# Performance work log

Measured on AMD Instinct MI355X. Metric: run time of the kernel, lower is better.

Reference implementation:

```python
import jax, jax.numpy as jnp
import numpy as np

B, T, INPUT, HIDDEN = 64, 512, 512, 1024

def setup_inputs() -> dict:
    key = jax.random.key(0)
    ks = jax.random.split(key, 5)
    s_x = 1.0 / np.sqrt(INPUT)
    s_h = 1.0 / np.sqrt(HIDDEN)
    return {
        "x": jax.random.normal(ks[0], (B, T, INPUT), dtype=jnp.float32),
        "h_0": jnp.zeros((B, HIDDEN), dtype=jnp.float32),
        "Wx": jax.random.uniform(ks[1], (HIDDEN, INPUT), jnp.float32, -s_x, s_x),
        "bx": jax.random.uniform(ks[2], (HIDDEN,), jnp.float32, -s_x, s_x),
        "Wh": jax.random.uniform(ks[3], (HIDDEN, HIDDEN), jnp.float32, -s_h, s_h),
        "bh": jax.random.uniform(ks[4], (HIDDEN,), jnp.float32, -s_h, s_h),
    }

def reference(x, h_0, Wx, bx, Wh, bh):
    # Precompute input projection for all timesteps as one big GEMM: [B,T,H]
    x_proj = jnp.einsum('bti,hi->bth', x, Wx) + bx

    def step(h, xp_t):
        # pre-activation output stored; activated value carried forward (faithful to source)
        pre = xp_t + h @ Wh.T + bh        # [B,H]
        h_next = jnp.tanh(pre)
        return h_next, pre

    # scan over time: xs has leading T axis
    h_final, outs = jax.lax.scan(step, h_0, jnp.swapaxes(x_proj, 0, 1))
    outputs = jnp.swapaxes(outs, 0, 1)    # [B,T,H]
    return outputs, h_final
```

## Files before the change

### kernel.cpp

```cpp
#include <hip/hip_runtime.h>
#include <stdint.h>


typedef __attribute__((ext_vector_type(8))) short bf16x8;
typedef __attribute__((ext_vector_type(4))) float f32x4;

__device__ __forceinline__ uint32_t f2bf(float f) {
    union { float f; uint32_t u; } v; v.f = f;
    return (v.u + 0x7FFFu + ((v.u >> 16) & 1u)) >> 16;
}
__device__ __forceinline__ uint32_t pack2bf(float a, float b) {
    return f2bf(a) | (f2bf(b) << 16);
}
__device__ __forceinline__ float fast_tanh(float x) {
    const float xc = fminf(fmaxf(x, -15.f), 15.f);
    const float e  = __expf(2.f * xc);
    return (e - 1.f) * __builtin_amdgcn_rcpf(e + 1.f);
}

__global__ __launch_bounds__(256) void xproj_gemm(
    const float* __restrict__ x, const float* __restrict__ Wx,
    const float* __restrict__ bx, const float* __restrict__ bh,
    float* __restrict__ out)
{
    __shared__ __align__(16) uint8_t Ab[128 * 128];
    __shared__ __align__(16) uint8_t Bb[128 * 128];

    const int tid  = threadIdx.x;
    const int lane = tid & 63;
    const int wid  = tid >> 6;
    const int wm = wid >> 1, wn = wid & 1;
    const int m0 = (int)(blockIdx.x >> 3) * 128;
    const int n0 = (int)(blockIdx.x & 7) * 128;

    f32x4 acc[4][4];
    #pragma unroll
    for (int i = 0; i < 4; ++i)
        #pragma unroll
        for (int j = 0; j < 4; ++j) acc[i][j] = (f32x4){0.f, 0.f, 0.f, 0.f};

    const int sr = tid >> 4;
    const int sk = (tid & 15) << 2;

    for (int k0 = 0; k0 < 512; k0 += 64) {
        __syncthreads();
        #pragma unroll
        for (int p = 0; p < 8; ++p) {
            const int r = sr + p * 16;
            const float4 a = *(const float4*)(x  + (size_t)(m0 + r) * 512 + k0 + sk);
            const float4 b = *(const float4*)(Wx + (size_t)(n0 + r) * 512 + k0 + sk);
            const int byo = r * 128 + ((sk << 1) ^ ((r & 7) << 4));
            *(uint2*)(Ab + byo) = make_uint2(pack2bf(a.x, a.y), pack2bf(a.z, a.w));
            *(uint2*)(Bb + byo) = make_uint2(pack2bf(b.x, b.y), pack2bf(b.z, b.w));
        }
        __syncthreads();
        #pragma unroll
        for (int kt = 0; kt < 2; ++kt) {
            bf16x8 af[4], bfr[4];
            const int kb = (kt << 6) + ((lane >> 4) << 4);
            #pragma unroll
            for (int q = 0; q < 4; ++q) {
                const int ar = wm * 64 + q * 16 + (lane & 15);
                const int br = wn * 64 + q * 16 + (lane & 15);
                af[q]  = *(const bf16x8*)(Ab + ar * 128 + (kb ^ ((ar & 7) << 4)));
                bfr[q] = *(const bf16x8*)(Bb + br * 128 + (kb ^ ((br & 7) << 4)));
            }
            #pragma unroll
            for (int mt = 0; mt < 4; ++mt)
                #pragma unroll
                for (int nt = 0; nt < 4; ++nt)
                    acc[mt][nt] = __builtin_amdgcn_mfma_f32_16x16x32_bf16(
                        af[mt], bfr[nt], acc[mt][nt], 0, 0, 0);
        }
    }

    #pragma unroll
    for (int nt = 0; nt < 4; ++nt) {
        const int n = n0 + wn * 64 + nt * 16 + (lane & 15);
        const float bias = bx[n] + bh[n];
        #pragma unroll
        for (int mt = 0; mt < 4; ++mt) {
            const int mb = m0 + wm * 64 + mt * 16 + ((lane >> 4) << 2);
            #pragma unroll
            for (int i = 0; i < 4; ++i)
                out[(size_t)(mb + i) * 1024 + n] = acc[mt][nt][i] + bias;
        }
    }
}

__global__ __launch_bounds__(512, 1) void rnn_scan(
    const float* __restrict__ h0, const float* __restrict__ Wh,
    float* __restrict__ out, float* __restrict__ hfin,
    uint32_t* __restrict__ hbuf)
{
    __shared__ __align__(16) uint8_t htile[2][49152];

    const int tid  = threadIdx.x;
    const int lane = tid & 63;
    const int wid  = tid >> 6;
    const int g    = (int)blockIdx.x & 7;
    const int nb   = (int)blockIdx.x >> 3;
    const int gb0  = g * 8;
    const int col  = nb * 128 + wid * 16 + (lane & 15);
    const int r4b  = ((lane >> 4) & 1) << 2;

    bf16x8 whf[32];
    {
        const float* wp = Wh + (size_t)col * 1024 + ((lane >> 4) << 3);
        #pragma unroll
        for (int kt = 0; kt < 32; ++kt) {
            const float4 w0 = *(const float4*)(wp + kt * 32);
            const float4 w1 = *(const float4*)(wp + kt * 32 + 4);
            bf16x8 f;
            f[0] = (short)f2bf(w0.x); f[1] = (short)f2bf(w0.y);
            f[2] = (short)f2bf(w0.z); f[3] = (short)f2bf(w0.w);
            f[4] = (short)f2bf(w1.x); f[5] = (short)f2bf(w1.y);
            f[6] = (short)f2bf(w1.z); f[7] = (short)f2bf(w1.w);
            whf[kt] = f;
        }
    }

    {
        const int colI = nb * 128 + lane * 2;
        const uint32_t u0 = f2bf(h0[(size_t)(gb0 + wid) * 1024 + colI]);
        const uint32_t u1 = f2bf(h0[(size_t)(gb0 + wid) * 1024 + colI + 1]);
        const int idx = (gb0 + wid) * 1024 + colI;
        __hip_atomic_store(&hbuf[idx],     (u0 << 16) | 1u, __ATOMIC_RELAXED, __HIP_MEMORY_SCOPE_AGENT);
        __hip_atomic_store(&hbuf[idx + 1], (u1 << 16) | 1u, __ATOMIC_RELAXED, __HIP_MEMORY_SCOPE_AGENT);
        *(uint32_t*)(htile[0] + wid * 2048 + ((colI * 2) ^ (wid << 4))) = u0 | (u1 << 16);
    }

    const int pb  = wid;
    const int pc0 = lane * 2;
    int ridx[7];
    #pragma unroll
    for (int r = 0; r < 7; ++r) {
        const int rbk = (nb + 1 + r) & 7;
        ridx[r] = (gb0 + pb) * 1024 + rbk * 128 + pc0;
    }

    float xpv[4];
    #pragma unroll
    for (int i = 0; i < 4; ++i)
        xpv[i] = out[((size_t)(gb0 + r4b + i) * 512 + 0) * 1024 + col];

    for (int t = 0; t < 512; ++t) {
        const int cur = t & 1;
        uint32_t* const src = hbuf + cur * 65536;
        uint32_t* const dst = hbuf + (cur ^ 1) * 65536;
        const uint32_t exptag = (uint32_t)(t + 1);
        const uint32_t ntag   = exptag + 1;

        uint32_t v[14];
        int rounds = 0;
        while (true) {
            #pragma unroll
            for (int r = 0; r < 7; ++r) {
                v[2 * r]     = __hip_atomic_load(&src[ridx[r]],     __ATOMIC_RELAXED, __HIP_MEMORY_SCOPE_AGENT);
                v[2 * r + 1] = __hip_atomic_load(&src[ridx[r] + 1], __ATOMIC_RELAXED, __HIP_MEMORY_SCOPE_AGENT);
            }
            bool ok = true;
            #pragma unroll
            for (int p = 0; p < 14; ++p) ok &= ((v[p] & 0xFFFFu) == exptag);
            if (ok) break;
            if (++rounds > 256) __builtin_amdgcn_s_sleep(2);
        }
        #pragma unroll
        for (int r = 0; r < 7; ++r) {
            const int rbk = (nb + 1 + r) & 7;
            const int c0  = rbk * 128 + pc0;
            const uint32_t pk = (v[2 * r] >> 16) | (v[2 * r + 1] & 0xFFFF0000u);
            *(uint32_t*)(htile[cur] + pb * 2048 + ((c0 * 2) ^ (pb << 4))) = pk;
        }
        __syncthreads();

        float xnext[4];
        if (t < 511) {
            #pragma unroll
            for (int i = 0; i < 4; ++i)
                xnext[i] = out[((size_t)(gb0 + r4b + i) * 512 + (t + 1)) * 1024 + col];
        }

        f32x4 a0 = (f32x4){0.f,0.f,0.f,0.f}, a1 = a0, a2 = a0, a3 = a0;
        {
            const int b_  = lane & 7;
            const int kbx = (lane >> 4) << 4;
            const int swz = b_ << 4;
            const uint8_t* hb = htile[cur] + b_ * 2048;
            #pragma unroll
            for (int kt = 0; kt < 32; kt += 4) {
                const bf16x8 f0 = *(const bf16x8*)(hb + (((kt    ) * 64 + kbx) ^ swz));
                const bf16x8 f1 = *(const bf16x8*)(hb + (((kt + 1) * 64 + kbx) ^ swz));
                const bf16x8 f2 = *(const bf16x8*)(hb + (((kt + 2) * 64 + kbx) ^ swz));
                const bf16x8 f3 = *(const bf16x8*)(hb + (((kt + 3) * 64 + kbx) ^ swz));
                a0 = __builtin_amdgcn_mfma_f32_16x16x32_bf16(f0, whf[kt    ], a0, 0, 0, 0);
                a1 = __builtin_amdgcn_mfma_f32_16x16x32_bf16(f1, whf[kt + 1], a1, 0, 0, 0);
                a2 = __builtin_amdgcn_mfma_f32_16x16x32_bf16(f2, whf[kt + 2], a2, 0, 0, 0);
                a3 = __builtin_amdgcn_mfma_f32_16x16x32_bf16(f3, whf[kt + 3], a3, 0, 0, 0);
            }
        }

        float pre[4], hn[4];
        #pragma unroll
        for (int i = 0; i < 4; ++i) {
            pre[i] = ((a0[i] + a1[i]) + (a2[i] + a3[i])) + xpv[i];
            hn[i]  = fast_tanh(pre[i]);
        }
        if (lane < 32) {
            if (t < 511) {
                uint32_t hu[4];
                #pragma unroll
                for (int i = 0; i < 4; ++i) hu[i] = f2bf(hn[i]);
                #pragma unroll
                for (int i = 0; i < 4; ++i)
                    __hip_atomic_store(&dst[(gb0 + r4b + i) * 1024 + col], (hu[i] << 16) | ntag,
                                       __ATOMIC_RELAXED, __HIP_MEMORY_SCOPE_AGENT);
                #pragma unroll
                for (int i = 0; i < 4; ++i)
                    *(uint16_t*)(htile[cur ^ 1] + (r4b + i) * 2048 + ((col * 2) ^ ((r4b + i) << 4))) = (uint16_t)hu[i];
            }
        } else {
            #pragma unroll
            for (int i = 0; i < 4; ++i) {
                out[((size_t)(gb0 + r4b + i) * 512 + t) * 1024 + col] = pre[i];
                if (t == 511) hfin[(size_t)(gb0 + r4b + i) * 1024 + col] = hn[i];
            }
        }
        #pragma unroll
        for (int i = 0; i < 4; ++i) xpv[i] = xnext[i];
    }
}

extern "C" void kernel_launch(void* const* d_in, const int* in_sizes, int n_in,
                              void* d_out, int out_size, void* d_ws, size_t ws_size,
                              hipStream_t stream) {
    const float* x   = (const float*)d_in[0];
    const float* h0_ = (const float*)d_in[1];
    const float* Wx  = (const float*)d_in[2];
    const float* bx  = (const float*)d_in[3];
    const float* Wh  = (const float*)d_in[4];
    const float* bh  = (const float*)d_in[5];
    float* out  = (float*)d_out;
    float* hfin = out + (size_t)64 * 512 * 1024;
    uint32_t* hbuf = (uint32_t*)d_ws;

    hipMemsetAsync(d_ws, 0xFF, (size_t)2 * 64 * 1024 * sizeof(uint32_t), stream);

    xproj_gemm<<<dim3(2048), dim3(256), 0, stream>>>(x, Wx, bx, bh, out);
    rnn_scan<<<dim3(64), dim3(512), 0, stream>>>(h0_, Wh, out, hfin, hbuf);
}
```

Before: 1.562 ms.

## Remap h-exchange polling to per-wave column blocks with 64-bit loads

Changes how each wave polls the tagged hidden-state buffer. Each non-zero wave now owns one remote column block across 8 batch rows and reads it with eight 64-bit atomic loads per lane, replacing 14 scattered 32-bit loads per lane. Wave 0, whose block is local, skips polling. A double-buffered load/check loop keeps one round of loads in flight while the previous round's tags are checked, to cut spin latency. The lane-to-data mapping is more complex, and wrong indexing or tag masking would produce incorrect results or deadlock.

```diff
diff --git a/kernel.cpp b/kernel.cpp
--- a/kernel.cpp
+++ b/kernel.cpp
@@ -4,6 +4,7 @@
 
 typedef __attribute__((ext_vector_type(8))) short bf16x8;
 typedef __attribute__((ext_vector_type(4))) float f32x4;
+typedef unsigned long long u64;
 
 __device__ __forceinline__ uint32_t f2bf(float f) {
     union { float f; uint32_t u; } v; v.f = f;
@@ -130,14 +131,13 @@
         *(uint32_t*)(htile[0] + wid * 2048 + ((colI * 2) ^ (wid << 4))) = u0 | (u1 << 16);
     }
 
-    const int pb  = wid;
-    const int pc0 = lane * 2;
-    int ridx[7];
-    #pragma unroll
-    for (int r = 0; r < 7; ++r) {
-        const int rbk = (nb + 1 + r) & 7;
-        ridx[r] = (gb0 + pb) * 1024 + rbk * 128 + pc0;
-    }
+    const int rbk = (nb + wid) & 7;
+    const int bl  = lane >> 3;
+    const int c8  = (lane & 7) << 4;
+    const int ib  = (gb0 + bl) * 1024 + rbk * 128 + c8;
+    const int sbase = bl * 2048;
+    const int soff  = rbk * 256 + ((lane & 7) << 5);
+    const int sxor  = bl << 4;
 
     float xpv[4];
     #pragma unroll
@@ -150,27 +150,45 @@
         uint32_t* const dst = hbuf + (cur ^ 1) * 65536;
         const uint32_t exptag = (uint32_t)(t + 1);
         const uint32_t ntag   = exptag + 1;
-
-        uint32_t v[14];
-        int rounds = 0;
-        while (true) {
-            #pragma unroll
-            for (int r = 0; r < 7; ++r) {
-                v[2 * r]     = __hip_atomic_load(&src[ridx[r]],     __ATOMIC_RELAXED, __HIP_MEMORY_SCOPE_AGENT);
-                v[2 * r + 1] = __hip_atomic_load(&src[ridx[r] + 1], __ATOMIC_RELAXED, __HIP_MEMORY_SCOPE_AGENT);
-            }
-            bool ok = true;
-            #pragma unroll
-            for (int p = 0; p < 14; ++p) ok &= ((v[p] & 0xFFFFu) == exptag);
-            if (ok) break;
-            if (++rounds > 256) __builtin_amdgcn_s_sleep(2);
-        }
-        #pragma unroll
-        for (int r = 0; r < 7; ++r) {
-            const int rbk = (nb + 1 + r) & 7;
-            const int c0  = rbk * 128 + pc0;
-            const uint32_t pk = (v[2 * r] >> 16) | (v[2 * r + 1] & 0xFFFF0000u);
-            *(uint32_t*)(htile[cur] + pb * 2048 + ((c0 * 2) ^ (pb << 4))) = pk;
+        const u64 tag2 = ((u64)exptag << 32) | (u64)exptag;
+
+        if (wid > 0) {
+            u64 va[8], vb[8];
+            #pragma unroll
+            for (int j = 0; j < 8; ++j)
+                va[j] = __hip_atomic_load((const u64*)&src[ib + 2 * j],
+                                          __ATOMIC_RELAXED, __HIP_MEMORY_SCOPE_AGENT);
+            const u64* w = va;
+            int rounds = 0;
+            while (true) {
+                #pragma unroll
+                for (int j = 0; j < 8; ++j)
+                    vb[j] = __hip_atomic_load((const u64*)&src[ib + 2 * j],
+                                              __ATOMIC_RELAXED, __HIP_MEMORY_SCOPE_AGENT);
+                bool ok = true;
+                #pragma unroll
+                for (int j = 0; j < 8; ++j)
+                    ok &= (((va[j] ^ tag2) & 0x0000FFFF0000FFFFull) == 0);
+                if (ok) { w = va; break; }
+
+                #pragma unroll
+                for (int j = 0; j < 8; ++j)
+                    va[j] = __hip_atomic_load((const u64*)&src[ib + 2 * j],
+                                              __ATOMIC_RELAXED, __HIP_MEMORY_SCOPE_AGENT);
+                ok = true;
+                #pragma unroll
+                for (int j = 0; j < 8; ++j)
+                    ok &= (((vb[j] ^ tag2) & 0x0000FFFF0000FFFFull) == 0);
+                if (ok) { w = vb; break; }
+                if (++rounds > 512) __builtin_amdgcn_s_sleep(2);
+            }
+            #pragma unroll
+            for (int j = 0; j < 8; ++j) {
+                const uint32_t lo = (uint32_t)w[j];
+                const uint32_t hi = (uint32_t)(w[j] >> 32);
+                const uint32_t pk = (lo >> 16) | (hi & 0xFFFF0000u);
+                *(uint32_t*)(htile[cur] + sbase + ((soff + 4 * j) ^ sxor)) = pk;
+            }
         }
         __syncthreads();
 
```

New measurement: 3.705 ms. +137.2%, slower.

## Add per-block flag polling before loading tagged hidden-state values

Applied to the files above, without the earlier changes.

Each block now publishes one flag per step after all of its tagged hidden-state stores have drained (waitcnt plus a block barrier). Consumers spin on seven per-producer flags, one per lane, instead of repeatedly reloading fourteen tagged data words, then read the data once and keep the tag check as a fallback. The next-step xproj prefetch moves after the output stores. The aim is lighter polling traffic on the critical cross-block handoff, at the cost of an extra barrier and a memory drain on every step.

```diff
diff --git a/kernel.cpp b/kernel.cpp
--- a/kernel.cpp
+++ b/kernel.cpp
@@ -91,7 +91,8 @@
 __global__ __launch_bounds__(512, 1) void rnn_scan(
     const float* __restrict__ h0, const float* __restrict__ Wh,
     float* __restrict__ out, float* __restrict__ hfin,
-    uint32_t* __restrict__ hbuf)
+    uint32_t* __restrict__ hbuf,
+    uint32_t* __restrict__ tagb)
 {
     __shared__ __align__(16) uint8_t htile[2][49152];
 
@@ -128,6 +129,11 @@
         __hip_atomic_store(&hbuf[idx],     (u0 << 16) | 1u, __ATOMIC_RELAXED, __HIP_MEMORY_SCOPE_AGENT);
         __hip_atomic_store(&hbuf[idx + 1], (u1 << 16) | 1u, __ATOMIC_RELAXED, __HIP_MEMORY_SCOPE_AGENT);
         *(uint32_t*)(htile[0] + wid * 2048 + ((colI * 2) ^ (wid << 4))) = u0 | (u1 << 16);
+        asm volatile("s_waitcnt vmcnt(0)" ::: "memory");
+        __syncthreads();
+        if (tid == 0)
+            __hip_atomic_store(&tagb[((0 << 6) + (g << 3) + nb) << 4], 1u,
+                               __ATOMIC_RELAXED, __HIP_MEMORY_SCOPE_AGENT);
     }
 
     const int pb  = wid;
@@ -138,6 +144,8 @@
         const int rbk = (nb + 1 + r) & 7;
         ridx[r] = (gb0 + pb) * 1024 + rbk * 128 + pc0;
     }
+    const int myrbk  = (nb + 1 + (lane < 7 ? lane : 0)) & 7;
+    const int tbase  = ((g << 3) + myrbk) << 4;
 
     float xpv[4];
     #pragma unroll
@@ -151,19 +159,38 @@
         const uint32_t exptag = (uint32_t)(t + 1);
         const uint32_t ntag   = exptag + 1;
 
+        {
+            const uint32_t* tp = &tagb[(cur << 10) + tbase];
+            int rounds = 0;
+            while (true) {
+                uint32_t tv = exptag;
+                if (lane < 7)
+                    tv = __hip_atomic_load(tp, __ATOMIC_RELAXED, __HIP_MEMORY_SCOPE_AGENT);
+                if (__all(tv == exptag)) break;
+                if (++rounds > 256) __builtin_amdgcn_s_sleep(2);
+            }
+        }
+
         uint32_t v[14];
-        int rounds = 0;
-        while (true) {
+        {
             #pragma unroll
             for (int r = 0; r < 7; ++r) {
                 v[2 * r]     = __hip_atomic_load(&src[ridx[r]],     __ATOMIC_RELAXED, __HIP_MEMORY_SCOPE_AGENT);
                 v[2 * r + 1] = __hip_atomic_load(&src[ridx[r] + 1], __ATOMIC_RELAXED, __HIP_MEMORY_SCOPE_AGENT);
             }
-            bool ok = true;
-            #pragma unroll
-            for (int p = 0; p < 14; ++p) ok &= ((v[p] & 0xFFFFu) == exptag);
-            if (ok) break;
-            if (++rounds > 256) __builtin_amdgcn_s_sleep(2);
+            int rounds = 0;
+            while (true) {
+                bool ok = true;
+                #pragma unroll
+                for (int p = 0; p < 14; ++p) ok &= ((v[p] & 0xFFFFu) == exptag);
+                if (ok) break;
+                #pragma unroll
+                for (int r = 0; r < 7; ++r) {
+                    v[2 * r]     = __hip_atomic_load(&src[ridx[r]],     __ATOMIC_RELAXED, __HIP_MEMORY_SCOPE_AGENT);
+                    v[2 * r + 1] = __hip_atomic_load(&src[ridx[r] + 1], __ATOMIC_RELAXED, __HIP_MEMORY_SCOPE_AGENT);
+                }
+                if (++rounds > 256) __builtin_amdgcn_s_sleep(2);
+            }
         }
         #pragma unroll
         for (int r = 0; r < 7; ++r) {
@@ -173,13 +200,6 @@
             *(uint32_t*)(htile[cur] + pb * 2048 + ((c0 * 2) ^ (pb << 4))) = pk;
         }
         __syncthreads();
-
-        float xnext[4];
-        if (t < 511) {
-            #pragma unroll
-            for (int i = 0; i < 4; ++i)
-                xnext[i] = out[((size_t)(gb0 + r4b + i) * 512 + (t + 1)) * 1024 + col];
-        }
 
         f32x4 a0 = (f32x4){0.f,0.f,0.f,0.f}, a1 = a0, a2 = a0, a3 = a0;
         {
@@ -206,8 +226,8 @@
             pre[i] = ((a0[i] + a1[i]) + (a2[i] + a3[i])) + xpv[i];
             hn[i]  = fast_tanh(pre[i]);
         }
-        if (lane < 32) {
-            if (t < 511) {
+        if (t < 511) {
+            if (lane < 32) {
                 uint32_t hu[4];
                 #pragma unroll
                 for (int i = 0; i < 4; ++i) hu[i] = f2bf(hn[i]);
@@ -219,15 +239,27 @@
                 for (int i = 0; i < 4; ++i)
                     *(uint16_t*)(htile[cur ^ 1] + (r4b + i) * 2048 + ((col * 2) ^ ((r4b + i) << 4))) = (uint16_t)hu[i];
             }
-        } else {
+            asm volatile("s_waitcnt vmcnt(0)" ::: "memory");
+            __syncthreads();
+            if (tid == 0)
+                __hip_atomic_store(&tagb[(((cur ^ 1) << 6) + (g << 3) + nb) << 4], ntag,
+                                   __ATOMIC_RELAXED, __HIP_MEMORY_SCOPE_AGENT);
+        }
+        if (lane >= 32) {
             #pragma unroll
             for (int i = 0; i < 4; ++i) {
                 out[((size_t)(gb0 + r4b + i) * 512 + t) * 1024 + col] = pre[i];
                 if (t == 511) hfin[(size_t)(gb0 + r4b + i) * 1024 + col] = hn[i];
             }
         }
-        #pragma unroll
-        for (int i = 0; i < 4; ++i) xpv[i] = xnext[i];
+        if (t < 511) {
+            float xnext[4];
+            #pragma unroll
+            for (int i = 0; i < 4; ++i)
+                xnext[i] = out[((size_t)(gb0 + r4b + i) * 512 + (t + 1)) * 1024 + col];
+            #pragma unroll
+            for (int i = 0; i < 4; ++i) xpv[i] = xnext[i];
+        }
     }
 }
 
@@ -242,10 +274,13 @@
     const float* bh  = (const float*)d_in[5];
     float* out  = (float*)d_out;
     float* hfin = out + (size_t)64 * 512 * 1024;
+
     uint32_t* hbuf = (uint32_t*)d_ws;
-
-    hipMemsetAsync(d_ws, 0xFF, (size_t)2 * 64 * 1024 * sizeof(uint32_t), stream);
+    uint32_t* tagb = hbuf + 2 * 65536;
+
+    hipMemsetAsync(d_ws, 0xFF,
+                   ((size_t)2 * 65536 + 2048) * sizeof(uint32_t), stream);
 
     xproj_gemm<<<dim3(2048), dim3(256), 0, stream>>>(x, Wx, bx, bh, out);
-    rnn_scan<<<dim3(64), dim3(512), 0, stream>>>(h0_, Wh, out, hfin, hbuf);
-}
+    rnn_scan<<<dim3(64), dim3(512), 0, stream>>>(h0_, Wh, out, hfin, hbuf, tagb);
+}
```

New measurement: 1.942 ms. +24.3%, slower.
